# Kernel tuning notes

Measured on AMD Instinct MI355X. Metric: run time of the kernel, lower is better.

## Reference

```python
import jax, jax.numpy as jnp
import numpy as np

N_U = 20000; N_I = 20000; D = 256
NNZ = 600000; EGG = 300000; EDD = 300000; B = 8192
DROP = 0.1; LAM2 = 1e-7


def _attention(x, W, a, edges):
    # GAT-style attention over sampled relationship edges (src -> tgt).
    n, d = x.shape
    h = x @ W                                  # [n, d]
    src, tgt = edges[0], edges[1]
    e = jax.nn.leaky_relu((h @ a[:d])[src] + (h @ a[d:])[tgt], 0.2)  # [E]
    m = jax.ops.segment_max(e, tgt, num_segments=n)
    m = jnp.where(jnp.isfinite(m), m, 0.0)
    ex = jnp.exp(e - m[tgt])
    denom = jax.ops.segment_sum(ex, tgt, num_segments=n)             # [n]
    num = jax.ops.segment_sum(ex[:, None] * h[src], tgt, num_segments=n)  # [n, d]
    return num / (denom[:, None] + 1e-9)


def _spmm(rows, cols, vals, x, n_out):
    # sparse [n_out, n_in] @ dense [n_in, d]
    return jax.ops.segment_sum(vals[:, None] * x[cols], rows, num_segments=n_out)


def _mlp(x, W1, b1, W2, b2, W3, b3):
    h = jax.nn.relu(x @ W1 + b1)
    h = jax.nn.relu(h @ W2 + b2)
    return (h @ W3 + b3)[..., 0]


def setup_inputs() -> dict:
    key = jax.random.key(0)
    ks = jax.random.split(key, 24)
    s = 0.02
    inp = {
        'E_g_0': jax.random.normal(ks[0], (N_U, D), jnp.float32) * s,
        'E_d_0': jax.random.normal(ks[1], (N_I, D), jnp.float32) * s,
        'att_W': jax.random.normal(ks[2], (D, D), jnp.float32) * s,
        'att_a': jax.random.normal(ks[3], (2 * D,), jnp.float32) * s,
        'att1_W': jax.random.normal(ks[4], (D, D), jnp.float32) * s,
        'att1_a': jax.random.normal(ks[5], (2 * D,), jnp.float32) * s,
        'W1': jax.random.normal(ks[6], (2 * D, D), jnp.float32) * s,
        'b1': jnp.zeros((D,), jnp.float32),
        'W2': jax.random.normal(ks[7], (D, D), jnp.float32) * s,
        'b2': jnp.zeros((D,), jnp.float32),
        'W3': jax.random.normal(ks[8], (D, 1), jnp.float32) * s,
        'b3': jnp.zeros((1,), jnp.float32),
        'M1': jax.random.normal(ks[9], (2 * D, D), jnp.float32) * s,
        'mb1': jnp.zeros((D,), jnp.float32),
        'M2': jax.random.normal(ks[10], (D, D), jnp.float32) * s,
        'mb2': jnp.zeros((D,), jnp.float32),
        'adj_vals': jax.random.uniform(ks[11], (NNZ,), jnp.float32),
        'uids': jax.random.randint(ks[12], (B,), 0, N_U, jnp.int32),
        'iids': jax.random.randint(ks[13], (B,), 0, N_I, jnp.int32),
        'pos': jax.random.randint(ks[14], (B,), 0, N_I, jnp.int32),
        'neg': jax.random.randint(ks[15], (B,), 0, N_I, jnp.int32),
        'gene_edges': jax.random.randint(ks[16], (2, EGG), 0, N_U, jnp.int32),
        'drug_edges': jax.random.randint(ks[17], (2, EDD), 0, N_I, jnp.int32),
        'adj_rows': jax.random.randint(ks[18], (NNZ,), 0, N_U, jnp.int32),
        'adj_cols': jax.random.randint(ks[19], (NNZ,), 0, N_I, jnp.int32),
        'drop1': jax.random.bernoulli(ks[20], 1.0 - DROP, (NNZ,)),
        'drop2': jax.random.bernoulli(ks[21], 1.0 - DROP, (NNZ,)),
    }
    return inp


def reference(E_g_0, E_d_0, att_W, att_a, att1_W, att1_a, W1, b1, W2, b2, W3, b3,
              M1, mb1, M2, mb2, adj_vals, uids, iids, pos, neg,
              gene_edges, drug_edges, adj_rows, adj_cols, drop1, drop2):
    # Attention-modulated layer-0 embeddings
    E_d0 = 0.1 * _attention(E_d_0, att_W, att_a, drug_edges) + E_d_0
    E_g0 = 0.1 * _attention(E_g_0, att_W, att_a, gene_edges) + E_g_0

    # sparse_dropout + spmm (two independent dropout draws, as in the source)
    scale = 1.0 / (1.0 - DROP)
    v1 = adj_vals * drop1.astype(adj_vals.dtype) * scale
    v2 = adj_vals * drop2.astype(adj_vals.dtype) * scale
    E_g = _spmm(adj_rows, adj_cols, v1, E_d0, N_U)   # adj @ E_d0
    E_d = _spmm(adj_cols, adj_rows, v2, E_g0, N_I)   # adj.T @ E_g0

    u = E_g[uids]; p = E_d[pos]; ng = E_d[neg]
    pos_s = _mlp(jnp.concatenate([u, p], axis=-1), W1, b1, W2, b2, W3, b3)
    neg_s = _mlp(jnp.concatenate([u, ng], axis=-1), W1, b1, W2, b2, W3, b3)

    # BCE-with-logits (labels 1 for pos, 0 for neg) + BPR term
    loss_pos = jnp.mean(jax.nn.softplus(-pos_s))
    loss_neg = jnp.mean(jax.nn.softplus(neg_s))
    loss_bpr = jnp.mean(jax.nn.softplus(-(pos_s - neg_s)))
    loss_r = loss_pos + loss_neg + loss_bpr

    params = (E_g_0, E_d_0, att_W, att_a, att1_W, att1_a,
              W1, b1, W2, b2, W3, b3, M1, mb1, M2, mb2)
    loss_reg = LAM2 * sum(jnp.sum(p_ * p_) for p_ in params)

    loss = loss_reg + loss_r  # loss_s == 0
    return jnp.stack([loss, loss_r, jnp.zeros((), loss.dtype)])
```

## Files before the change

kernel.cpp:

```cpp
#include <hip/hip_runtime.h>
#include <math.h>

#define N_NODES 20000
#define D       256
#define NNZ     600000
#define NEDGE   300000
#define BATCH   8192
#define DROP_SCALE (1.0f/0.9f)
#define LAM2_F  1e-7f

#define M_PAD   20096
#define CSTRIDE 20032

#define C_ATT 56
#define C_ADJ 80

#define BINW 320
#define NBIN 63
#define TILE_E 2048
#define EPT 8
#define T_ATT ((NEDGE + TILE_E - 1) / TILE_E)
#define T_ADJ ((NNZ + TILE_E - 1) / TILE_E)
#define NBLK_P1 (2 * T_ATT + 2 * T_ADJ)
#define CAP_BIN_ATT 5376
#define CAP_BIN_ADJ 9216

#define FP8_SCALE 256.0f
#define VSCALE    58980.0f
#define INV_VSCALE (1.0f/58980.0f)

typedef unsigned short u16;
typedef unsigned char  u8;
typedef __attribute__((ext_vector_type(8))) short bf16x8;
typedef __attribute__((ext_vector_type(4))) float f32x4;
typedef __attribute__((ext_vector_type(2))) float f32x2;
typedef __attribute__((ext_vector_type(4))) unsigned v4u;

__device__ inline float wave_reduce(float v) {
    #pragma unroll
    for (int off = 32; off > 0; off >>= 1) v += __shfl_down(v, off, 64);
    return v;
}

__device__ inline float softplus_f(float x) {
    float r = log1pf(__expf(-fabsf(x)));
    return x > 0.f ? x + r : r;
}

__device__ inline u16 f2bf(float f) {
    unsigned u = __float_as_uint(f);
    unsigned r = u + 0x7fff + ((u >> 16) & 1);
    return (u16)(r >> 16);
}
__device__ inline float bf2f(u16 b) { return __uint_as_float(((unsigned)b) << 16); }

__device__ inline u16 f2h(float f) {
    _Float16 h = (_Float16)f;
    return __builtin_bit_cast(u16, h);
}
__device__ inline float h2f(u16 b) {
    return (float)__builtin_bit_cast(_Float16, b);
}

__device__ inline unsigned f32x4_to_fp8x4(float a, float b, float c, float d) {
    int r = 0;
    r = __builtin_amdgcn_cvt_pk_fp8_f32(a, b, r, false);
    r = __builtin_amdgcn_cvt_pk_fp8_f32(c, d, r, true);
    return (unsigned)r;
}
__device__ inline u8 f32_to_fp8(float a) {
    int r = __builtin_amdgcn_cvt_pk_fp8_f32(a, a, 0, false);
    return (u8)(r & 0xff);
}

__device__ inline void gld_lds16(const void* g, void* l) {
    __builtin_amdgcn_global_load_lds((const __attribute__((address_space(1))) void*)g,
                                     (__attribute__((address_space(3))) void*)l, 16, 0, 0);
}

struct RegArgs { const float* p[14]; int n[14]; };

__device__ inline void gemm_tile_k(const u16* __restrict__ A, const u16* __restrict__ BT, int K,
                                   int bm, int bn, short (*As)[32], short (*Bs)[32],
                                   f32x4 (&acr)[4][4]) {
    int tid = threadIdx.x, wave = tid >> 6, lane = tid & 63;
    int sr = lane >> 2, sc = (lane & 3) * 8;
    int wr = (wave >> 1) * 64, wc = (wave & 1) * 64;
    int fr = lane & 15, fk = (lane >> 4) * 8;
    for (int k0 = 0; k0 < K; k0 += 32) {
        #pragma unroll
        for (int j = 0; j < 2; j++) {
            int r0 = wave * 32 + j * 16;
            gld_lds16(A  + (size_t)(bm + r0 + sr) * K + k0 + sc, &As[r0][0]);
            gld_lds16(BT + (size_t)(bn + r0 + sr) * K + k0 + sc, &Bs[r0][0]);
        }
        __syncthreads();
        bf16x8 af[4], bfr[4];
        #pragma unroll
        for (int i = 0; i < 4; i++) af[i]  = *(const bf16x8*)&As[wr + i*16 + fr][fk];
        #pragma unroll
        for (int j = 0; j < 4; j++) bfr[j] = *(const bf16x8*)&Bs[wc + j*16 + fr][fk];
        #pragma unroll
        for (int i = 0; i < 4; i++)
            #pragma unroll
            for (int j = 0; j < 4; j++)
                acr[i][j] = __builtin_amdgcn_mfma_f32_16x16x32_bf16(af[i], bfr[j], acr[i][j], 0, 0, 0);
        __syncthreads();
    }
}

__global__ __launch_bounds__(1024) void init_kernel(const float* __restrict__ att_W,
                                                    const float* __restrict__ att_a,
                                                    float* __restrict__ wlv, float* __restrict__ wrv,
                                                    int* __restrict__ zbase, int zwords) {
    int tid = threadIdx.x;
    for (int i = tid; i < zwords; i += 1024) zbase[i] = 0;
    int t = tid & 255, q = tid >> 8;
    float s1 = 0.f, s2 = 0.f;
    for (int n = q * 64; n < q * 64 + 64; n++) {
        float w = att_W[(size_t)t * D + n];
        s1 += w * att_a[n];
        s2 += w * att_a[D + n];
    }
    __shared__ float r1[4][256], r2[4][256];
    r1[q][t] = s1; r2[q][t] = s2;
    __syncthreads();
    if (q == 0) {
        wlv[t] = r1[0][t] + r1[1][t] + r1[2][t] + r1[3][t];
        wrv[t] = r2[0][t] + r2[1][t] + r2[2][t] + r2[3][t];
    }
}

#define NB_CAST (2 * M_PAD / 4)
#define NB_T1   (D * D / 256)
#define NB_T2   (2 * D * D / 256)
#define NB_T3   (D * D / 256)
#define NB_PREP (NB_CAST + NB_T1 + NB_T2 + NB_T3)
#define NB_REG  448
__global__ __launch_bounds__(256) void p1prep_kernel(
        const int* __restrict__ dtgt, const int* __restrict__ dsrc,
        const int* __restrict__ gtgt, const int* __restrict__ gsrc,
        const int* __restrict__ ar,   const int* __restrict__ ac,
        const float* __restrict__ vals,
        const void* __restrict__ drop1, const void* __restrict__ drop2,
        int* __restrict__ pcur, unsigned* __restrict__ attbin, uint2* __restrict__ adjbin,
        const float* __restrict__ E_g, const float* __restrict__ E_d,
        u16* __restrict__ Eg_bf, u16* __restrict__ Ed_bf,
        const float* __restrict__ att_W,
        const float* __restrict__ W1, const float* __restrict__ W2,
        u16* __restrict__ attWT, u16* __restrict__ W1T, u16* __restrict__ W2T,
        const float* __restrict__ wlv, const float* __restrict__ wrv,
        float* __restrict__ hl_g, float* __restrict__ hr_g,
        float* __restrict__ hl_d, float* __restrict__ hr_d,
        float* __restrict__ regp, RegArgs ra, float* __restrict__ acc) {
    if (blockIdx.x < NBLK_P1) {
        __shared__ int hist[NBIN];
        __shared__ int basep[NBIN];
        for (int i = threadIdx.x; i < NBIN; i += 256) hist[i] = 0;
        __syncthreads();

        int b = blockIdx.x;
        int s, t0;
        if (b < T_ATT)               { s = 0; t0 = b; }
        else if (b < 2 * T_ATT)      { s = 1; t0 = b - T_ATT; }
        else if (b < 2*T_ATT + T_ADJ){ s = 2; t0 = b - 2 * T_ATT; }
        else                         { s = 3; t0 = b - 2 * T_ATT - T_ADJ; }
        int base = t0 * TILE_E;
        int regN = (s < 2) ? NEDGE : NNZ;

        int bins[EPT], rank[EPT];
        unsigned key[EPT], pay[EPT];
        float pv[EPT];

        if (s < 2) {
            const int* tgt = (s == 0) ? dtgt : gtgt;
            const int* src = (s == 0) ? dsrc : gsrc;
            #pragma unroll
            for (int e = 0; e < EPT; e++) {
                int idx = base + e * 256 + threadIdx.x;
                rank[e] = -1;
                if (idx < regN) {
                    int k = __builtin_nontemporal_load(tgt + idx);
                    int sv = __builtin_nontemporal_load(src + idx);
                    key[e] = (unsigned)k; pay[e] = (unsigned)sv;
                    bins[e] = k / BINW;
                    rank[e] = atomicAdd(&hist[bins[e]], 1);
                }
            }
        } else {
            const int* keyp = (s == 2) ? ar : ac;
            const int* othp = (s == 2) ? ac : ar;
            const void* drp = (s == 2) ? drop1 : drop2;
            bool nzs = ((const u8*)drp)[4 * threadIdx.x + 1] != 0;
            const bool bf = __popcll(__ballot(nzs)) > 16;
            #pragma unroll
            for (int e = 0; e < EPT; e++) {
                int idx = base + e * 256 + threadIdx.x;
                rank[e] = -1;
                if (idx < regN) {
                    bool keep = bf ? (__builtin_nontemporal_load((const u8*)drp + idx) != 0)
                                   : (__builtin_nontemporal_load((const unsigned*)drp + idx) != 0);
                    if (keep) {
                        int k = __builtin_nontemporal_load(keyp + idx);
                        float v = __builtin_nontemporal_load(vals + idx) * DROP_SCALE;
                        int oth = __builtin_nontemporal_load(othp + idx);
                        key[e] = (unsigned)k; pay[e] = (unsigned)oth; pv[e] = v;
                        bins[e] = k / BINW;
                        rank[e] = atomicAdd(&hist[bins[e]], 1);
                    }
                }
            }
        }
        __syncthreads();
        for (int i = threadIdx.x; i < NBIN; i += 256) {
            int h = hist[i];
            basep[i] = h ? atomicAdd(&pcur[s * NBIN + i], h) : 0;
        }
        __syncthreads();
        if (s < 2) {
            unsigned* seg = attbin + (size_t)s * NBIN * CAP_BIN_ATT;
            #pragma unroll
            for (int e = 0; e < EPT; e++) {
                if (rank[e] < 0) continue;
                int pos = basep[bins[e]] + rank[e];
                if (pos < CAP_BIN_ATT)
                    seg[(size_t)bins[e] * CAP_BIN_ATT + pos] = key[e] | (pay[e] << 16);
            }
        } else {
            uint2* seg = adjbin + (size_t)(s - 2) * NBIN * CAP_BIN_ADJ;
            #pragma unroll
            for (int e = 0; e < EPT; e++) {
                if (rank[e] < 0) continue;
                int pos = basep[bins[e]] + rank[e];
                if (pos < CAP_BIN_ADJ) {
                    uint2 pr; pr.x = key[e] | (pay[e] << 16); pr.y = __float_as_uint(pv[e]);
                    seg[(size_t)bins[e] * CAP_BIN_ADJ + pos] = pr;
                }
            }
        }
    } else {
        int bid = blockIdx.x - NBLK_P1;
        int w = threadIdx.x >> 6, lane = threadIdx.x & 63;
        if (bid < NB_CAST) {
            int wid  = (bid * 256 + threadIdx.x) >> 6;
            int is_d = (wid >= M_PAD);
            int row  = is_d ? wid - M_PAD : wid;
            u16* dst = (is_d ? Ed_bf : Eg_bf) + (size_t)row * D;
            float s3 = 0.f;
            if (row >= N_NODES) {
                ((ushort4*)dst)[lane] = make_ushort4(0, 0, 0, 0);
            } else {
                const float* src = (is_d ? E_d : E_g) + (size_t)row * D;
                float4 e  = ((const float4*)src)[lane];
                float4 l4 = ((const float4*)wlv)[lane];
                float4 r4 = ((const float4*)wrv)[lane];
                ((ushort4*)dst)[lane] = make_ushort4(f2bf(e.x), f2bf(e.y), f2bf(e.z), f2bf(e.w));
                float s1 = e.x*l4.x + e.y*l4.y + e.z*l4.z + e.w*l4.w;
                float s2 = e.x*r4.x + e.y*r4.y + e.z*r4.z + e.w*r4.w;
                s3 = e.x*e.x + e.y*e.y + e.z*e.z + e.w*e.w;
                s1 = wave_reduce(s1); s2 = wave_reduce(s2);
                if (lane == 0) {
                    if (is_d) { hl_d[row] = s1; hr_d[row] = s2; }
                    else      { hl_g[row] = s1; hr_g[row] = s2; }
                }
            }
            s3 = wave_reduce(s3);
            __shared__ float sm3[4];
            if (lane == 0) sm3[threadIdx.x >> 6] = s3;
            __syncthreads();
            if (threadIdx.x == 0) regp[bid] = sm3[0] + sm3[1] + sm3[2] + sm3[3];
        } else if (bid < NB_CAST + NB_T1) {
            int o = (bid - NB_CAST) * 256 + threadIdx.x;
            int n = o >> 8, k = o & 255;
            attWT[o] = f2bf(att_W[(size_t)k * D + n]);
        } else if (bid < NB_CAST + NB_T1 + NB_T2) {
            int o = (bid - NB_CAST - NB_T1) * 256 + threadIdx.x;
            int n = o / (2 * D), k = o - n * (2 * D);
            W1T[o] = f2bf(W1[(size_t)k * D + n]);
        } else if (bid < NB_PREP) {
            int o = (bid - NB_CAST - NB_T1 - NB_T2) * 256 + threadIdx.x;
            int n = o >> 8, k = o & 255;
            W2T[o] = f2bf(W2[(size_t)k * D + n]);
        } else {
            int rb = bid - NB_PREP;
            const float* p = ra.p[rb >> 5];
            int n = ra.n[rb >> 5];
            int base = (rb & 31) * 4096;
            if (base >= n) return;
            float sum = 0.f;
            if (base + 4096 <= n) {
                const float4* p4 = (const float4*)(p + base);
                float4 v = p4[threadIdx.x];
                sum += v.x*v.x + v.y*v.y + v.z*v.z + v.w*v.w;
                v = p4[256 + threadIdx.x];
                sum += v.x*v.x + v.y*v.y + v.z*v.z + v.w*v.w;
                v = p4[512 + threadIdx.x];
                sum += v.x*v.x + v.y*v.y + v.z*v.z + v.w*v.w;
                v = p4[768 + threadIdx.x];
                sum += v.x*v.x + v.y*v.y + v.z*v.z + v.w*v.w;
            } else {
                for (int i = base + threadIdx.x; i < n; i += 256) { float v = p[i]; sum += v * v; }
            }
            sum = wave_reduce(sum);
            __shared__ float smr[4];
            if (lane == 0) smr[w] = sum;
            __syncthreads();
            if (threadIdx.x == 0)
                atomicAdd(&acc[0], smr[0] + smr[1] + smr[2] + smr[3]);
        }
    }
}

#define NB_P2   (4 * NBIN)
#define NB_ATTG ((M_PAD / 128) * 4)
__global__ __launch_bounds__(256) void p2gemm_kernel(
        const int* __restrict__ pcur, const unsigned* __restrict__ attbin,
        const uint2* __restrict__ adjbin,
        const float* __restrict__ hl_d, const float* __restrict__ hr_d,
        const float* __restrict__ hl_g, const float* __restrict__ hr_g,
        int* __restrict__ cnt, unsigned* __restrict__ srcs, unsigned* __restrict__ adj,
        const u16* __restrict__ Eg_bf, const u16* __restrict__ Ed_bf,
        const u16* __restrict__ attWT, u8* __restrict__ h_g, u8* __restrict__ h_d) {
    if (blockIdx.x < NB_P2) {
        int s   = blockIdx.x / NBIN;
        int bin = blockIdx.x - s * NBIN;
        int nodeBase = bin * BINW;
        __shared__ int cur[BINW];
        for (int t = threadIdx.x; t < BINW; t += 256) cur[t] = 0;
        __syncthreads();
        if (s < 2) {
            int m = pcur[s * NBIN + bin]; if (m > CAP_BIN_ATT) m = CAP_BIN_ATT;
            const unsigned* seg = attbin + ((size_t)s * NBIN + bin) * CAP_BIN_ATT;
            const float* hl = (s == 0) ? hl_d : hl_g;
            const float* hr = (s == 0) ? hr_d : hr_g;
            for (int k = threadIdx.x; k < m; k += 256) {
                unsigned e = seg[k];
                int lk  = (int)(e & 0xFFFFu) - nodeBase;
                int src = (int)(e >> 16);
                float ev = hl[src] + hr[nodeBase + lk];
                ev = ev > 0.f ? ev : 0.2f * ev;
                u16 xh = f2h(__expf(ev));
                int c = atomicAdd(&cur[lk], 1);
                if (c < C_ATT)
                    srcs[(size_t)s * N_NODES * C_ATT + (size_t)(nodeBase + lk) * C_ATT + c] =
                        (unsigned)src | ((unsigned)xh << 16);
            }
            __syncthreads();
            for (int t = threadIdx.x; t < BINW; t += 256) {
                int node = nodeBase + t;
                if (node < N_NODES) {
                    int n = cur[t]; if (n > C_ATT) n = C_ATT;
                    cnt[s * CSTRIDE + node] = n;
                }
            }
        } else {
            int m = pcur[s * NBIN + bin]; if (m > CAP_BIN_ADJ) m = CAP_BIN_ADJ;
            const uint2* seg = adjbin + ((size_t)(s - 2) * NBIN + bin) * CAP_BIN_ADJ;
            for (int k = threadIdx.x; k < m; k += 256) {
                uint2 e = seg[k];
                int lk  = (int)(e.x & 0xFFFFu) - nodeBase;
                int oth = (int)(e.x >> 16);
                float v = __uint_as_float(e.y);
                unsigned pk = ((unsigned)(v * VSCALE + 0.5f) << 16) | (unsigned)oth;
                int c = atomicAdd(&cur[lk], 1);
                if (c < C_ADJ)
                    adj[(size_t)(s - 2) * N_NODES * C_ADJ + (size_t)(nodeBase + lk) * C_ADJ + c] = pk;
            }
            __syncthreads();
            for (int t = threadIdx.x; t < BINW; t += 256) {
                int node = nodeBase + t;
                if (node < N_NODES) {
                    int n = cur[t]; if (n > C_ADJ) n = C_ADJ;
                    cnt[s * CSTRIDE + node] = n;
                }
            }
        }
    } else {
        int t  = blockIdx.x - NB_P2;
        int z  = t / (2 * (M_PAD / 128));
        int r  = t - z * (2 * (M_PAD / 128));
        int by = r / (M_PAD / 128);
        int bx = r - by * (M_PAD / 128);
        const u16* A = z ? Ed_bf : Eg_bf;
        u8* C = z ? h_d : h_g;
        __shared__ __align__(16) short As[128][32];
        __shared__ __align__(16) short Bs[128][32];
        int wave = threadIdx.x >> 6, lane = threadIdx.x & 63;
        int bm = bx * 128, bn = by * 128;
        f32x4 acr[4][4];
        #pragma unroll
        for (int i = 0; i < 4; i++)
            #pragma unroll
            for (int j = 0; j < 4; j++)
                #pragma unroll
                for (int q = 0; q < 4; q++) acr[i][j][q] = 0.f;
        gemm_tile_k(A, attWT, D, bm, bn, As, Bs, acr);
        int wr = (wave >> 1) * 64, wc = (wave & 1) * 64, fr = lane & 15;
        #pragma unroll
        for (int j = 0; j < 4; j++) {
            int col = bn + wc + j * 16 + fr;
            #pragma unroll
            for (int i = 0; i < 4; i++) {
                #pragma unroll
                for (int q = 0; q < 4; q++) {
                    int row = bm + wr + i * 16 + (lane >> 4) * 4 + q;
                    if (row < N_NODES)
                        C[(size_t)row * D + col] = f32_to_fp8(acr[i][j][q] * FP8_SCALE);
                }
            }
        }
    }
}

__global__ __launch_bounds__(256) void att_kernel(const u8* __restrict__ h_d, const u8* __restrict__ h_g,
                                                  const int* __restrict__ cur, const unsigned* __restrict__ srcs,
                                                  const u16* __restrict__ Ed_bf, const u16* __restrict__ Eg_bf,
                                                  u8* __restrict__ E_d0p, u8* __restrict__ E_g0p) {
    int wid  = (blockIdx.x * blockDim.x + threadIdx.x) >> 6;
    int lane = threadIdx.x & 63;
    if (wid >= 2 * N_NODES) return;
    int is_g = (wid >= N_NODES);
    int node = is_g ? wid - N_NODES : wid;
    const unsigned* h32 = (const unsigned*)(is_g ? h_g : h_d);
    int reg = is_g ? 1 : 0;
    const unsigned* sv = srcs + (size_t)reg * N_NODES * C_ATT + (size_t)node * C_ATT;
    int n = cur[reg * CSTRIDE + node];
    if (n > C_ATT) n = C_ATT;
    float ax = 0.f, ay = 0.f, az = 0.f, aw = 0.f, denom = 0.f;
    int k = 0;
    for (; k + 8 <= n; k += 8) {
        v4u qa = __builtin_nontemporal_load((const v4u*)(sv + k));
        v4u qb = __builtin_nontemporal_load((const v4u*)(sv + k + 4));
        unsigned g[8]; float x[8];
        #pragma unroll
        for (int j = 0; j < 4; j++) {
            g[j]     = h32[((size_t)(qa[j] & 0xFFFFu) << 6) + lane];
            g[4 + j] = h32[((size_t)(qb[j] & 0xFFFFu) << 6) + lane];
            x[j]     = h2f((u16)(qa[j] >> 16));
            x[4 + j] = h2f((u16)(qb[j] >> 16));
        }
        #pragma unroll
        for (int j = 0; j < 8; j++) {
            denom += x[j];
            f32x2 lo = __builtin_amdgcn_cvt_pk_f32_fp8(g[j], false);
            f32x2 hi = __builtin_amdgcn_cvt_pk_f32_fp8(g[j], true);
            ax += x[j]*lo[0]; ay += x[j]*lo[1]; az += x[j]*hi[0]; aw += x[j]*hi[1];
        }
    }
    for (; k + 4 <= n; k += 4) {
        v4u qa = __builtin_nontemporal_load((const v4u*)(sv + k));
        unsigned g[4]; float x[4];
        #pragma unroll
        for (int j = 0; j < 4; j++) {
            g[j] = h32[((size_t)(qa[j] & 0xFFFFu) << 6) + lane];
            x[j] = h2f((u16)(qa[j] >> 16));
        }
        #pragma unroll
        for (int j = 0; j < 4; j++) {
            denom += x[j];
            f32x2 lo = __builtin_amdgcn_cvt_pk_f32_fp8(g[j], false);
            f32x2 hi = __builtin_amdgcn_cvt_pk_f32_fp8(g[j], true);
            ax += x[j]*lo[0]; ay += x[j]*lo[1]; az += x[j]*hi[0]; aw += x[j]*hi[1];
        }
    }
    for (; k < n; k++) {
        unsigned q = sv[k];
        float xv = h2f((u16)(q >> 16));
        unsigned g = h32[((size_t)(q & 0xFFFFu) << 6) + lane];
        denom += xv;
        f32x2 lo = __builtin_amdgcn_cvt_pk_f32_fp8(g, false);
        f32x2 hi = __builtin_amdgcn_cvt_pk_f32_fp8(g, true);
        ax += xv*lo[0]; ay += xv*lo[1]; az += xv*hi[0]; aw += xv*hi[1];
    }
    float sc = 0.1f / (denom + 1e-9f);
    const u16* E0b = is_g ? Eg_bf : Ed_bf;
    u8*       out  = is_g ? E_g0p : E_d0p;
    ushort4 b4 = ((const ushort4*)(E0b + (size_t)node * D))[lane];
    unsigned pk = f32x4_to_fp8x4(FP8_SCALE * bf2f(b4.x) + sc * ax, FP8_SCALE * bf2f(b4.y) + sc * ay,
                                 FP8_SCALE * bf2f(b4.z) + sc * az, FP8_SCALE * bf2f(b4.w) + sc * aw);
    ((unsigned*)(out + (size_t)node * D))[lane] = pk;
}

__global__ __launch_bounds__(256) void pull_kernel(const int* __restrict__ uids, const int* __restrict__ pos,
                                                   const int* __restrict__ neg,
                                                   const int* __restrict__ cur, const unsigned* __restrict__ adj,
                                                   const u8* __restrict__ E_d0p, const u8* __restrict__ E_g0p,
                                                   u16* __restrict__ X) {
    int wid  = (blockIdx.x * blockDim.x + threadIdx.x) >> 6;
    int lane = threadIdx.x & 63;
    if (wid >= 3 * BATCH) return;
    int type = wid >> 13;
    int b    = wid & (BATCH - 1);
    int node, reg; const u8* E;
    if (type == 0)      { node = uids[b]; reg = 2; E = E_d0p; }
    else if (type == 1) { node = pos[b];  reg = 3; E = E_g0p; }
    else                { node = neg[b];  reg = 3; E = E_g0p; }
    const unsigned* E32 = (const unsigned*)E;
    const unsigned* av = adj + (size_t)(reg - 2) * N_NODES * C_ADJ + (size_t)node * C_ADJ;
    int n = cur[reg * CSTRIDE + node];
    if (n > C_ADJ) n = C_ADJ;
    float ax = 0.f, ay = 0.f, az = 0.f, aw = 0.f;
    int k = 0;
    for (; k + 8 <= n; k += 8) {
        v4u qa = __builtin_nontemporal_load((const v4u*)(av + k));
        v4u qb = __builtin_nontemporal_load((const v4u*)(av + k + 4));
        unsigned g[8]; float v[8];
        #pragma unroll
        for (int j = 0; j < 4; j++) {
            g[j]     = E32[((size_t)(qa[j] & 0xFFFFu) << 6) + lane];
            g[4 + j] = E32[((size_t)(qb[j] & 0xFFFFu) << 6) + lane];
            v[j]     = (float)(qa[j] >> 16) * INV_VSCALE;
            v[4 + j] = (float)(qb[j] >> 16) * INV_VSCALE;
        }
        #pragma unroll
        for (int j = 0; j < 8; j++) {
            f32x2 lo = __builtin_amdgcn_cvt_pk_f32_fp8(g[j], false);
            f32x2 hi = __builtin_amdgcn_cvt_pk_f32_fp8(g[j], true);
            ax += v[j]*lo[0]; ay += v[j]*lo[1]; az += v[j]*hi[0]; aw += v[j]*hi[1];
        }
    }
    for (; k + 4 <= n; k += 4) {
        v4u qa = __builtin_nontemporal_load((const v4u*)(av + k));
        unsigned g[4]; float v[4];
        #pragma unroll
        for (int j = 0; j < 4; j++) {
            g[j] = E32[((size_t)(qa[j] & 0xFFFFu) << 6) + lane];
            v[j] = (float)(qa[j] >> 16) * INV_VSCALE;
        }
        #pragma unroll
        for (int j = 0; j < 4; j++) {
            f32x2 lo = __builtin_amdgcn_cvt_pk_f32_fp8(g[j], false);
            f32x2 hi = __builtin_amdgcn_cvt_pk_f32_fp8(g[j], true);
            ax += v[j]*lo[0]; ay += v[j]*lo[1]; az += v[j]*hi[0]; aw += v[j]*hi[1];
        }
    }
    for (; k < n; k++) {
        unsigned q = av[k];
        int c = q & 0xFFFF;
        float v = (float)(q >> 16) * INV_VSCALE;
        unsigned g = E32[((size_t)c << 6) + lane];
        f32x2 lo = __builtin_amdgcn_cvt_pk_f32_fp8(g, false);
        f32x2 hi = __builtin_amdgcn_cvt_pk_f32_fp8(g, true);
        ax += v*lo[0]; ay += v*lo[1]; az += v*hi[0]; aw += v*hi[1];
    }
    const float inv = 1.0f / FP8_SCALE;
    ushort4 r = make_ushort4(f2bf(ax * inv), f2bf(ay * inv), f2bf(az * inv), f2bf(aw * inv));
    if (type == 0) {
        ((ushort4*)(X + (size_t)b * 2 * D))[lane] = r;
        ((ushort4*)(X + (size_t)(BATCH + b) * 2 * D))[lane] = r;
    } else if (type == 1) {
        ((ushort4*)(X + (size_t)b * 2 * D + D))[lane] = r;
    } else {
        ((ushort4*)(X + (size_t)(BATCH + b) * 2 * D + D))[lane] = r;
    }
}

#define MLP_NB (256 + 128 + 16)
__global__ __launch_bounds__(256) void mlp_kernel(
        const u16* __restrict__ X, const u16* __restrict__ W1T,
        u16* __restrict__ H1, const u16* __restrict__ W2T,
        const float* __restrict__ b1, const float* __restrict__ b2,
        const float* __restrict__ W3, const float* __restrict__ b3p,
        const float* __restrict__ regp, float* __restrict__ sbuf,
        float* __restrict__ acc, int* __restrict__ syn, float* __restrict__ out) {
    int bid = blockIdx.x, tid = threadIdx.x;
    int wave = tid >> 6, lane = tid & 63;
    __shared__ __align__(16) short As[128][32];
    __shared__ __align__(16) short Bs[128][32];
    __shared__ float sacc[128];
    if (bid < 256) {
        int bx = bid & 127, by = bid >> 7;
        int bm = bx * 128, bn = by * 128;
        f32x4 acr[4][4];
        #pragma unroll
        for (int i = 0; i < 4; i++)
            #pragma unroll
            for (int j = 0; j < 4; j++)
                #pragma unroll
                for (int q = 0; q < 4; q++) acr[i][j][q] = 0.f;
        gemm_tile_k(X, W1T, 2 * D, bm, bn, As, Bs, acr);
        int wr = (wave >> 1) * 64, wc = (wave & 1) * 64, fr = lane & 15;
        #pragma unroll
        for (int j = 0; j < 4; j++) {
            int col = bn + wc + j * 16 + fr;
            float bv = b1[col];
            #pragma unroll
            for (int i = 0; i < 4; i++) {
                #pragma unroll
                for (int q = 0; q < 4; q++) {
                    int row = bm + wr + i * 16 + (lane >> 4) * 4 + q;
                    H1[(size_t)row * D + col] = f2bf(fmaxf(acr[i][j][q] + bv, 0.f));
                }
            }
        }
        __threadfence();
        if (tid == 0) atomicAdd(&syn[bx], 1);
    } else if (bid < 384) {
        int x = bid - 256, bm = x * 128;
        if (tid == 0) {
            while (__hip_atomic_load(&syn[x], __ATOMIC_ACQUIRE, __HIP_MEMORY_SCOPE_AGENT) < 2)
                __builtin_amdgcn_s_sleep(8);
        }
        __syncthreads();
        for (int t = tid; t < 128; t += 256) sacc[t] = 0.f;
        __syncthreads();
        int wr = (wave >> 1) * 64, wc = (wave & 1) * 64, fr = lane & 15;
        for (int bn = 0; bn < 256; bn += 128) {
            f32x4 acr[4][4];
            #pragma unroll
            for (int i = 0; i < 4; i++)
                #pragma unroll
                for (int j = 0; j < 4; j++)
                    #pragma unroll
                    for (int q = 0; q < 4; q++) acr[i][j][q] = 0.f;
            gemm_tile_k(H1, W2T, D, bm, bn, As, Bs, acr);
            float bvj[4], w3j[4];
            #pragma unroll
            for (int j = 0; j < 4; j++) {
                int col = bn + wc + j * 16 + fr;
                bvj[j] = b2[col];
                w3j[j] = W3[col];
            }
            #pragma unroll
            for (int i = 0; i < 4; i++) {
                #pragma unroll
                for (int q = 0; q < 4; q++) {
                    float rs = 0.f;
                    #pragma unroll
                    for (int j = 0; j < 4; j++)
                        rs += fmaxf(acr[i][j][q] + bvj[j], 0.f) * w3j[j];
                    rs += __shfl_xor(rs, 1, 64);
                    rs += __shfl_xor(rs, 2, 64);
                    rs += __shfl_xor(rs, 4, 64);
                    rs += __shfl_xor(rs, 8, 64);
                    if (fr == 0)
                        atomicAdd(&sacc[wr + i * 16 + (lane >> 4) * 4 + q], rs);
                }
            }
            __syncthreads();
        }
        for (int t = tid; t < 128; t += 256) sbuf[bm + t] = sacc[t];
        __threadfence();
        if (tid == 0) atomicAdd(&syn[128], 1);
    } else {
        int tb = bid - 384;
        if (tid == 0) {
            while (__hip_atomic_load(&syn[128], __ATOMIC_ACQUIRE, __HIP_MEMORY_SCOPE_AGENT) < 128)
                __builtin_amdgcn_s_sleep(16);
        }
        __syncthreads();
        float b3 = b3p[0];
        float lp = 0.f, ln = 0.f, lb = 0.f, rsum = 0.f;
        for (int i = tb * 256 + tid; i < BATCH; i += 16 * 256) {
            float ps = sbuf[i] + b3, ns = sbuf[BATCH + i] + b3;
            lp += softplus_f(-ps);
            ln += softplus_f(ns);
            lb += softplus_f(-(ps - ns));
        }
        for (int i = tb * 256 + tid; i < NB_CAST; i += 16 * 256) rsum += regp[i];
        lp = wave_reduce(lp); ln = wave_reduce(ln); lb = wave_reduce(lb); rsum = wave_reduce(rsum);
        __shared__ float sm[4][4];
        if (lane == 0) { sm[0][wave] = lp; sm[1][wave] = ln; sm[2][wave] = lb; sm[3][wave] = rsum; }
        __syncthreads();
        if (tid == 0) {
            float a = 0.f, b = 0.f, c = 0.f, rg = 0.f;
            for (int i = 0; i < 4; i++) { a += sm[0][i]; b += sm[1][i]; c += sm[2][i]; rg += sm[3][i]; }
            atomicAdd(&acc[1], a); atomicAdd(&acc[2], b); atomicAdd(&acc[3], c);
            atomicAdd(&acc[0], rg);
        }
        __syncthreads();
        __shared__ int lastf;
        if (tid == 0) {
            __threadfence();
            int t = atomicAdd(&syn[129], 1);
            lastf = (t == 15);
        }
        __syncthreads();
        if (!lastf || tid != 0) return;
        float a0 = __hip_atomic_load(&acc[0], __ATOMIC_RELAXED, __HIP_MEMORY_SCOPE_AGENT);
        float a1 = __hip_atomic_load(&acc[1], __ATOMIC_RELAXED, __HIP_MEMORY_SCOPE_AGENT);
        float a2 = __hip_atomic_load(&acc[2], __ATOMIC_RELAXED, __HIP_MEMORY_SCOPE_AGENT);
        float a3 = __hip_atomic_load(&acc[3], __ATOMIC_RELAXED, __HIP_MEMORY_SCOPE_AGENT);
        float lr = (a1 + a2 + a3) * (1.0f / (float)BATCH);
        out[0] = LAM2_F * a0 + lr;
        out[1] = lr;
        out[2] = 0.f;
    }
}

extern "C" void kernel_launch(void* const* d_in, const int* in_sizes, int n_in,
                              void* d_out, int out_size, void* d_ws, size_t ws_size,
                              hipStream_t stream) {
    (void)n_in; (void)out_size; (void)ws_size;
    const float* E_g_0   = (const float*)d_in[0];
    const float* E_d_0   = (const float*)d_in[1];
    const float* att_W   = (const float*)d_in[2];
    const float* att_a   = (const float*)d_in[3];
    const float* W1      = (const float*)d_in[6];
    const float* b1      = (const float*)d_in[7];
    const float* W2      = (const float*)d_in[8];
    const float* b2      = (const float*)d_in[9];
    const float* W3      = (const float*)d_in[10];
    const float* b3      = (const float*)d_in[11];
    const float* adj_vals= (const float*)d_in[16];
    const int*   uids    = (const int*)d_in[17];
    const int*   pos     = (const int*)d_in[19];
    const int*   neg     = (const int*)d_in[20];
    const int*   gene_e  = (const int*)d_in[21];
    const int*   drug_e  = (const int*)d_in[22];
    const int*   adj_rows= (const int*)d_in[23];
    const int*   adj_cols= (const int*)d_in[24];
    const void*  drop1   = d_in[25];
    const void*  drop2   = d_in[26];

    char* ws = (char*)d_ws;
    size_t cur_off = 0;
    auto take = [&](size_t bytes) -> void* {
        void* p = ws + cur_off;
        cur_off += (bytes + 255) & ~(size_t)255;
        return p;
    };
    u16* Eg_bf = (u16*)take((size_t)M_PAD * D * 2);
    u16* Ed_bf = (u16*)take((size_t)M_PAD * D * 2);
    u16* X     = Eg_bf;
    u16* attWT = (u16*)take((size_t)D * D * 2);
    u16* W1T   = (u16*)take((size_t)D * 2 * D * 2);
    u16* W2T   = (u16*)take((size_t)D * D * 2);
    u8*  h_g   = (u8*)take((size_t)M_PAD * D);
    u8*  h_d   = (u8*)take((size_t)M_PAD * D);
    u8*  E_g0p = (u8*)take((size_t)N_NODES * D);
    u8*  E_d0p = (u8*)take((size_t)N_NODES * D);
    u16* H1    = (u16*)take((size_t)2 * BATCH * D * 2);
    float* hl_g = (float*)take((size_t)N_NODES * 4);
    float* hr_g = (float*)take((size_t)N_NODES * 4);
    float* hl_d = (float*)take((size_t)N_NODES * 4);
    float* hr_d = (float*)take((size_t)N_NODES * 4);
    float* wlv  = (float*)take((size_t)D * 4);
    float* wrv  = (float*)take((size_t)D * 4);
    float* regp = (float*)take((size_t)NB_CAST * 4);
    float* sbuf = (float*)take((size_t)2 * BATCH * 4);
    unsigned* srcs = (unsigned*)take((size_t)2 * N_NODES * C_ATT * 4);
    unsigned* adj  = (unsigned*)take((size_t)2 * N_NODES * C_ADJ * 4);
    int*   cnt  = (int*)take((size_t)4 * CSTRIDE * 4);
    unsigned* attbin = (unsigned*)take((size_t)2 * NBIN * CAP_BIN_ATT * 4);
    uint2*    adjbin = (uint2*)take((size_t)2 * NBIN * CAP_BIN_ADJ * 8);
    int*      pcur = (int*)take((size_t)4 * NBIN * 4);
    float*    acc  = (float*)take(256);
    int*      syn  = (int*)take(1024);
    int zwords = (int)((((char*)syn + 1024) - (char*)pcur) / 4);

    init_kernel<<<1, 1024, 0, stream>>>(att_W, att_a, wlv, wrv, pcur, zwords);

    RegArgs ra;
    for (int i = 0; i < 14; i++) { ra.p[i] = (const float*)d_in[i + 2]; ra.n[i] = in_sizes[i + 2]; }
    p1prep_kernel<<<NBLK_P1 + NB_PREP + NB_REG, 256, 0, stream>>>(
        drug_e + NEDGE, drug_e, gene_e + NEDGE, gene_e,
        adj_rows, adj_cols, adj_vals, drop1, drop2,
        pcur, attbin, adjbin,
        E_g_0, E_d_0, Eg_bf, Ed_bf, att_W, W1, W2,
        attWT, W1T, W2T, wlv, wrv, hl_g, hr_g, hl_d, hr_d, regp, ra, acc);

    p2gemm_kernel<<<NB_P2 + NB_ATTG, 256, 0, stream>>>(
        pcur, attbin, adjbin, hl_d, hr_d, hl_g, hr_g, cnt, srcs, adj,
        Eg_bf, Ed_bf, attWT, h_g, h_d);

    att_kernel<<<10000, 256, 0, stream>>>(h_d, h_g, cnt, srcs,
                                          Ed_bf, Eg_bf, E_d0p, E_g0p);

    pull_kernel<<<6144, 256, 0, stream>>>(uids, pos, neg, cnt, adj, E_d0p, E_g0p, X);

    mlp_kernel<<<MLP_NB, 256, 0, stream>>>(X, W1T, H1, W2T, b1, b2, W3, b3,
                                           regp, sbuf, acc, syn, (float*)d_out);
}
```

Measured before the change: 355.6 us.

## Split fused MLP kernel with spin-wait sync into separate GEMM and tail launches

Replaces the single persistent MLP kernel, which chained layer-1 GEMM, layer-2 GEMM and loss reduction through global atomic flags and spin-waits, with two generic bf16 GEMM launches and a small tail reduction kernel. The second GEMM now covers both column halves in parallel blocks and atomically adds partial W3 dot products into a zeroed score buffer, which the init kernel clears. This removes spin-waiting and serialized per-block column loops and gains parallelism in layer 2, at the cost of extra launch overhead and global float atomics.

Result: faster. 299.9 us (-15.7%).

```diff
diff --git a/kernel.cpp b/kernel.cpp
--- a/kernel.cpp
+++ b/kernel.cpp
@@ -412,6 +412,83 @@
     }
 }
 
+__global__ __launch_bounds__(256) void gemm_bf16(const u16* __restrict__ A, const u16* __restrict__ BT,
+                                                 void* __restrict__ C, int M, int N, int K,
+                                                 const float* __restrict__ bias, int do_relu, int out_mode,
+                                                 const float* __restrict__ w3) {
+    __shared__ __align__(16) short As[128][32];
+    __shared__ __align__(16) short Bs[128][32];
+    int tid = threadIdx.x;
+    int wave = tid >> 6, lane = tid & 63;
+    int bm = blockIdx.x * 128, bn = blockIdx.y * 128;
+
+    f32x4 acr[4][4];
+    #pragma unroll
+    for (int i = 0; i < 4; i++)
+        #pragma unroll
+        for (int j = 0; j < 4; j++)
+            #pragma unroll
+            for (int r = 0; r < 4; r++) acr[i][j][r] = 0.f;
+
+    gemm_tile_k(A, BT, K, bm, bn, As, Bs, acr);
+
+    int wr = (wave >> 1) * 64, wc = (wave & 1) * 64, fr = lane & 15;
+
+    if (out_mode == 2) {
+        __shared__ float sacc[128];
+        for (int t = tid; t < 128; t += 256) sacc[t] = 0.f;
+        __syncthreads();
+        float bvj[4], w3j[4];
+        #pragma unroll
+        for (int j = 0; j < 4; j++) {
+            int col = bn + wc + j * 16 + fr;
+            bvj[j] = bias[col];
+            w3j[j] = w3[col];
+        }
+        #pragma unroll
+        for (int i = 0; i < 4; i++) {
+            #pragma unroll
+            for (int r = 0; r < 4; r++) {
+                float rs = 0.f;
+                #pragma unroll
+                for (int j = 0; j < 4; j++) {
+                    float v = fmaxf(acr[i][j][r] + bvj[j], 0.f);
+                    rs += v * w3j[j];
+                }
+                rs += __shfl_xor(rs, 1, 64);
+                rs += __shfl_xor(rs, 2, 64);
+                rs += __shfl_xor(rs, 4, 64);
+                rs += __shfl_xor(rs, 8, 64);
+                if (fr == 0)
+                    atomicAdd(&sacc[wr + i * 16 + (lane >> 4) * 4 + r], rs);
+            }
+        }
+        __syncthreads();
+        float* sb = (float*)C;
+        for (int t = tid; t < 128; t += 256)
+            atomicAdd(&sb[bm + t], sacc[t]);
+        return;
+    }
+
+    #pragma unroll
+    for (int j = 0; j < 4; j++) {
+        int col = bn + wc + j * 16 + fr;
+        float bv = bias ? bias[col] : 0.f;
+        #pragma unroll
+        for (int i = 0; i < 4; i++) {
+            #pragma unroll
+            for (int r = 0; r < 4; r++) {
+                int row = bm + wr + i * 16 + (lane >> 4) * 4 + r;
+                if (row < M) {
+                    float v = acr[i][j][r] + bv;
+                    if (do_relu) v = fmaxf(v, 0.f);
+                    ((u16*)C)[(size_t)row * N + col] = f2bf(v);
+                }
+            }
+        }
+    }
+}
+
 __global__ __launch_bounds__(256) void att_kernel(const u8* __restrict__ h_d, const u8* __restrict__ h_g,
                                                   const int* __restrict__ cur, const unsigned* __restrict__ srcs,
                                                   const u16* __restrict__ Ed_bf, const u16* __restrict__ Eg_bf,
@@ -555,137 +632,49 @@
     }
 }
 
-#define MLP_NB (256 + 128 + 16)
-__global__ __launch_bounds__(256) void mlp_kernel(
-        const u16* __restrict__ X, const u16* __restrict__ W1T,
-        u16* __restrict__ H1, const u16* __restrict__ W2T,
-        const float* __restrict__ b1, const float* __restrict__ b2,
-        const float* __restrict__ W3, const float* __restrict__ b3p,
-        const float* __restrict__ regp, float* __restrict__ sbuf,
-        float* __restrict__ acc, int* __restrict__ syn, float* __restrict__ out) {
+#define NB_TAIL 16
+__global__ __launch_bounds__(256) void tail_kernel(const float* __restrict__ s,
+                                                   const float* __restrict__ b3p,
+                                                   const float* __restrict__ regp,
+                                                   float* __restrict__ acc, float* __restrict__ out) {
     int bid = blockIdx.x, tid = threadIdx.x;
-    int wave = tid >> 6, lane = tid & 63;
-    __shared__ __align__(16) short As[128][32];
-    __shared__ __align__(16) short Bs[128][32];
-    __shared__ float sacc[128];
-    if (bid < 256) {
-        int bx = bid & 127, by = bid >> 7;
-        int bm = bx * 128, bn = by * 128;
-        f32x4 acr[4][4];
-        #pragma unroll
-        for (int i = 0; i < 4; i++)
-            #pragma unroll
-            for (int j = 0; j < 4; j++)
-                #pragma unroll
-                for (int q = 0; q < 4; q++) acr[i][j][q] = 0.f;
-        gemm_tile_k(X, W1T, 2 * D, bm, bn, As, Bs, acr);
-        int wr = (wave >> 1) * 64, wc = (wave & 1) * 64, fr = lane & 15;
-        #pragma unroll
-        for (int j = 0; j < 4; j++) {
-            int col = bn + wc + j * 16 + fr;
-            float bv = b1[col];
-            #pragma unroll
-            for (int i = 0; i < 4; i++) {
-                #pragma unroll
-                for (int q = 0; q < 4; q++) {
-                    int row = bm + wr + i * 16 + (lane >> 4) * 4 + q;
-                    H1[(size_t)row * D + col] = f2bf(fmaxf(acr[i][j][q] + bv, 0.f));
-                }
-            }
-        }
+    int w = tid >> 6, lane = tid & 63;
+    float b3 = b3p[0];
+    float lp = 0.f, ln = 0.f, lb = 0.f, rsum = 0.f;
+    for (int i = bid * 256 + tid; i < BATCH; i += NB_TAIL * 256) {
+        float ps = s[i] + b3, ns = s[BATCH + i] + b3;
+        lp += softplus_f(-ps);
+        ln += softplus_f(ns);
+        lb += softplus_f(-(ps - ns));
+    }
+    for (int i = bid * 256 + tid; i < NB_CAST; i += NB_TAIL * 256) rsum += regp[i];
+    lp = wave_reduce(lp); ln = wave_reduce(ln); lb = wave_reduce(lb); rsum = wave_reduce(rsum);
+    __shared__ float sm[4][4];
+    if (lane == 0) { sm[0][w] = lp; sm[1][w] = ln; sm[2][w] = lb; sm[3][w] = rsum; }
+    __syncthreads();
+    if (tid == 0) {
+        float a = 0.f, b = 0.f, c = 0.f, rg = 0.f;
+        for (int i = 0; i < 4; i++) { a += sm[0][i]; b += sm[1][i]; c += sm[2][i]; rg += sm[3][i]; }
+        atomicAdd(&acc[1], a); atomicAdd(&acc[2], b); atomicAdd(&acc[3], c);
+        atomicAdd(&acc[0], rg);
+    }
+    __syncthreads();
+    __shared__ int lastf;
+    if (tid == 0) {
         __threadfence();
-        if (tid == 0) atomicAdd(&syn[bx], 1);
-    } else if (bid < 384) {
-        int x = bid - 256, bm = x * 128;
-        if (tid == 0) {
-            while (__hip_atomic_load(&syn[x], __ATOMIC_ACQUIRE, __HIP_MEMORY_SCOPE_AGENT) < 2)
-                __builtin_amdgcn_s_sleep(8);
-        }
-        __syncthreads();
-        for (int t = tid; t < 128; t += 256) sacc[t] = 0.f;
-        __syncthreads();
-        int wr = (wave >> 1) * 64, wc = (wave & 1) * 64, fr = lane & 15;
-        for (int bn = 0; bn < 256; bn += 128) {
-            f32x4 acr[4][4];
-            #pragma unroll
-            for (int i = 0; i < 4; i++)
-                #pragma unroll
-                for (int j = 0; j < 4; j++)
-                    #pragma unroll
-                    for (int q = 0; q < 4; q++) acr[i][j][q] = 0.f;
-            gemm_tile_k(H1, W2T, D, bm, bn, As, Bs, acr);
-            float bvj[4], w3j[4];
-            #pragma unroll
-            for (int j = 0; j < 4; j++) {
-                int col = bn + wc + j * 16 + fr;
-                bvj[j] = b2[col];
-                w3j[j] = W3[col];
-            }
-            #pragma unroll
-            for (int i = 0; i < 4; i++) {
-                #pragma unroll
-                for (int q = 0; q < 4; q++) {
-                    float rs = 0.f;
-                    #pragma unroll
-                    for (int j = 0; j < 4; j++)
-                        rs += fmaxf(acr[i][j][q] + bvj[j], 0.f) * w3j[j];
-                    rs += __shfl_xor(rs, 1, 64);
-                    rs += __shfl_xor(rs, 2, 64);
-                    rs += __shfl_xor(rs, 4, 64);
-                    rs += __shfl_xor(rs, 8, 64);
-                    if (fr == 0)
-                        atomicAdd(&sacc[wr + i * 16 + (lane >> 4) * 4 + q], rs);
-                }
-            }
-            __syncthreads();
-        }
-        for (int t = tid; t < 128; t += 256) sbuf[bm + t] = sacc[t];
-        __threadfence();
-        if (tid == 0) atomicAdd(&syn[128], 1);
-    } else {
-        int tb = bid - 384;
-        if (tid == 0) {
-            while (__hip_atomic_load(&syn[128], __ATOMIC_ACQUIRE, __HIP_MEMORY_SCOPE_AGENT) < 128)
-                __builtin_amdgcn_s_sleep(16);
-        }
-        __syncthreads();
-        float b3 = b3p[0];
-        float lp = 0.f, ln = 0.f, lb = 0.f, rsum = 0.f;
-        for (int i = tb * 256 + tid; i < BATCH; i += 16 * 256) {
-            float ps = sbuf[i] + b3, ns = sbuf[BATCH + i] + b3;
-            lp += softplus_f(-ps);
-            ln += softplus_f(ns);
-            lb += softplus_f(-(ps - ns));
-        }
-        for (int i = tb * 256 + tid; i < NB_CAST; i += 16 * 256) rsum += regp[i];
-        lp = wave_reduce(lp); ln = wave_reduce(ln); lb = wave_reduce(lb); rsum = wave_reduce(rsum);
-        __shared__ float sm[4][4];
-        if (lane == 0) { sm[0][wave] = lp; sm[1][wave] = ln; sm[2][wave] = lb; sm[3][wave] = rsum; }
-        __syncthreads();
-        if (tid == 0) {
-            float a = 0.f, b = 0.f, c = 0.f, rg = 0.f;
-            for (int i = 0; i < 4; i++) { a += sm[0][i]; b += sm[1][i]; c += sm[2][i]; rg += sm[3][i]; }
-            atomicAdd(&acc[1], a); atomicAdd(&acc[2], b); atomicAdd(&acc[3], c);
-            atomicAdd(&acc[0], rg);
-        }
-        __syncthreads();
-        __shared__ int lastf;
-        if (tid == 0) {
-            __threadfence();
-            int t = atomicAdd(&syn[129], 1);
-            lastf = (t == 15);
-        }
-        __syncthreads();
-        if (!lastf || tid != 0) return;
-        float a0 = __hip_atomic_load(&acc[0], __ATOMIC_RELAXED, __HIP_MEMORY_SCOPE_AGENT);
-        float a1 = __hip_atomic_load(&acc[1], __ATOMIC_RELAXED, __HIP_MEMORY_SCOPE_AGENT);
-        float a2 = __hip_atomic_load(&acc[2], __ATOMIC_RELAXED, __HIP_MEMORY_SCOPE_AGENT);
-        float a3 = __hip_atomic_load(&acc[3], __ATOMIC_RELAXED, __HIP_MEMORY_SCOPE_AGENT);
-        float lr = (a1 + a2 + a3) * (1.0f / (float)BATCH);
-        out[0] = LAM2_F * a0 + lr;
-        out[1] = lr;
-        out[2] = 0.f;
-    }
+        unsigned t = atomicAdd((unsigned*)&acc[8], 1u);
+        lastf = (t == NB_TAIL - 1);
+    }
+    __syncthreads();
+    if (!lastf || tid != 0) return;
+    float a0 = __hip_atomic_load(&acc[0], __ATOMIC_RELAXED, __HIP_MEMORY_SCOPE_AGENT);
+    float a1 = __hip_atomic_load(&acc[1], __ATOMIC_RELAXED, __HIP_MEMORY_SCOPE_AGENT);
+    float a2 = __hip_atomic_load(&acc[2], __ATOMIC_RELAXED, __HIP_MEMORY_SCOPE_AGENT);
+    float a3 = __hip_atomic_load(&acc[3], __ATOMIC_RELAXED, __HIP_MEMORY_SCOPE_AGENT);
+    float lr = (a1 + a2 + a3) * (1.0f / (float)BATCH);
+    out[0] = LAM2_F * a0 + lr;
+    out[1] = lr;
+    out[2] = 0.f;
 }
 
 extern "C" void kernel_launch(void* const* d_in, const int* in_sizes, int n_in,
@@ -738,7 +727,6 @@
     float* wlv  = (float*)take((size_t)D * 4);
     float* wrv  = (float*)take((size_t)D * 4);
     float* regp = (float*)take((size_t)NB_CAST * 4);
-    float* sbuf = (float*)take((size_t)2 * BATCH * 4);
     unsigned* srcs = (unsigned*)take((size_t)2 * N_NODES * C_ATT * 4);
     unsigned* adj  = (unsigned*)take((size_t)2 * N_NODES * C_ADJ * 4);
     int*   cnt  = (int*)take((size_t)4 * CSTRIDE * 4);
@@ -746,8 +734,8 @@
     uint2*    adjbin = (uint2*)take((size_t)2 * NBIN * CAP_BIN_ADJ * 8);
     int*      pcur = (int*)take((size_t)4 * NBIN * 4);
     float*    acc  = (float*)take(256);
-    int*      syn  = (int*)take(1024);
-    int zwords = (int)((((char*)syn + 1024) - (char*)pcur) / 4);
+    float*    sbuf = (float*)take((size_t)2 * BATCH * 4);
+    int zwords = (int)((((char*)sbuf + (size_t)2 * BATCH * 4) - (char*)pcur) / 4);
 
     init_kernel<<<1, 1024, 0, stream>>>(att_W, att_a, wlv, wrv, pcur, zwords);
 
@@ -769,6 +757,10 @@
 
     pull_kernel<<<6144, 256, 0, stream>>>(uids, pos, neg, cnt, adj, E_d0p, E_g0p, X);
 
-    mlp_kernel<<<MLP_NB, 256, 0, stream>>>(X, W1T, H1, W2T, b1, b2, W3, b3,
-                                           regp, sbuf, acc, syn, (float*)d_out);
-}
+    gemm_bf16<<<dim3(2 * BATCH / 128, 2, 1), 256, 0, stream>>>(
+        X, W1T, H1, 2 * BATCH, D, 2 * D, b1, 1, 0, nullptr);
+    gemm_bf16<<<dim3(2 * BATCH / 128, 2, 1), 256, 0, stream>>>(
+        H1, W2T, sbuf, 2 * BATCH, D, D, b2, 1, 2, W3);
+
+    tail_kernel<<<NB_TAIL, 256, 0, stream>>>(sbuf, b3, regp, acc, (float*)d_out);
+}
```
